# Optimization experiments

Measured on AMD Instinct MI355X. Metric: run time of the kernel, lower is better.

## Reference

```python
import jax, jax.numpy as jnp
import numpy as np

B, C_IN, C_OUT, N_LOW, N_UP, K = 16, 256, 128, 10242, 40962, 7  # ico order 5 -> 6, 1-ring size 7


def setup_inputs() -> dict:
    key = jax.random.key(0)
    k1, k2, k3 = jax.random.split(key, 3)
    x = jax.random.normal(k1, (B, C_IN, N_LOW), dtype=jnp.float32)
    # nn.Linear(in_feats, K*out_feats); stored as [in, K*out] for einsum
    weight = jax.random.normal(k2, (C_IN, K * C_OUT), dtype=jnp.float32) * 0.05
    bias = jax.random.normal(k3, (K * C_OUT,), dtype=jnp.float32) * 0.05
    # flat neighbor indices must cover every up-level vertex at least once
    rng = np.random.default_rng(0)
    cover = rng.permutation(N_UP)
    extra = rng.integers(0, N_UP, size=N_LOW * K - N_UP)
    neigh_flat = jnp.asarray(np.concatenate([cover, extra]).astype(np.int32))
    return {"x": x, "weight": weight, "bias": bias,
            "neigh_flat": neigh_flat, "n_up": N_UP}


def reference(x, weight, bias, neigh_flat, n_up):
    # x: [B, C_in, V] -> per-vertex linear expand to [B, V, K*C_out]
    Bn, _, V = x.shape
    y = jnp.einsum('bcv,cf->bvf', x, weight) + bias
    y = y.reshape(Bn, V * K, C_OUT)            # [B, V*K, C_out]
    y = jnp.transpose(y, (1, 0, 2))            # [V*K, B, C_out] segment axis first
    sums = jax.ops.segment_sum(y, neigh_flat, num_segments=n_up)      # [n_up, B, C_out]
    counts = jax.ops.segment_sum(jnp.ones((V * K,), y.dtype), neigh_flat,
                                 num_segments=n_up)                    # [n_up]
    out = sums / counts[:, None, None]         # mean over variable-size groups
    return jnp.transpose(out, (1, 2, 0))       # [B, C_out, n_up]
```

## Files before the change

kernel.cpp:

```cpp
#include <hip/hip_runtime.h>
#include <stdint.h>

#define B_    16
#define CIN   256
#define COUT  128
#define VLOW  10242
#define NUP   40962
#define KTAP  7
#define FTOT  (KTAP * COUT)
#define VK    (VLOW * KTAP)
#define NBLK  41
#define VPAD  10368
#define CSR_CAP 512

typedef __attribute__((ext_vector_type(4))) float  floatx4;
typedef __attribute__((ext_vector_type(8))) short  bf16x8;

typedef __attribute__((address_space(3))) unsigned char       lds_u8;
typedef const __attribute__((address_space(1))) unsigned char gbl_u8;

__device__ __forceinline__ void gl_lds16(const unsigned short* g, unsigned short* l) {
    __builtin_amdgcn_global_load_lds((gbl_u8*)g, (lds_u8*)l, 16, 0, 0);
}

__device__ __forceinline__ unsigned short f2bf(float f) {
    union { float f; unsigned int u; } x; x.f = f;
    unsigned int r = x.u + 0x7FFFu + ((x.u >> 16) & 1u);
    return (unsigned short)(r >> 16);
}
__device__ __forceinline__ float bflo(unsigned int u) {
    union { unsigned int u; float f; } x; x.u = u << 16; return x.f;
}
__device__ __forceinline__ float bfhi(unsigned int u) {
    union { unsigned int u; float f; } x; x.u = u & 0xFFFF0000u; return x.f;
}


__global__ void count_kernel(const int* __restrict__ neigh, int* __restrict__ counts) {
    int i = blockIdx.x * blockDim.x + threadIdx.x;
    if (i < VK) atomicAdd(&counts[neigh[i]], 1);
}

__global__ __launch_bounds__(1024)
void scan_local(const int* __restrict__ counts, int* __restrict__ offs, int* __restrict__ bsum) {
    __shared__ int s[1024];
    const int t = threadIdx.x;
    const int idx = blockIdx.x * 1024 + t;
    int v = (idx < NUP) ? counts[idx] : 0;
    s[t] = v;
    __syncthreads();
    int acc = v;
    for (int off = 1; off < 1024; off <<= 1) {
        int add = (t >= off) ? s[t - off] : 0;
        __syncthreads();
        acc += add;
        s[t] = acc;
        __syncthreads();
    }
    if (idx < NUP) offs[idx] = acc - v;
    if (t == 1023) bsum[blockIdx.x] = acc;
}

__global__ void scan_sums(const int* __restrict__ bsum, int* __restrict__ bbase) {
    __shared__ int s[64];
    int t = threadIdx.x;
    s[t] = (t < NBLK) ? bsum[t] : 0;
    __syncthreads();
    if (t == 0) {
        int r = 0;
        for (int j = 0; j < NBLK; ++j) { bbase[j] = r; r += s[j]; }
    }
}

__global__ void fill_csr(const int* __restrict__ neigh, const int* __restrict__ offs,
                         const int* __restrict__ bbase, int* __restrict__ cursor,
                         int* __restrict__ csr) {
    int i = blockIdx.x * blockDim.x + threadIdx.x;
    if (i < VK) {
        int n = neigh[i];
        int p = atomicAdd(&cursor[n], 1);
        csr[offs[n] + bbase[n >> 10] + p] = i;
    }
}

__global__ void make_pos(const int* __restrict__ offs, const int* __restrict__ bbase,
                         int* __restrict__ pos) {
    int i = blockIdx.x * blockDim.x + threadIdx.x;
    if (i <= NUP) pos[i] = (i < NUP) ? (offs[i] + bbase[i >> 10]) : VK;
}

__global__ __launch_bounds__(256)
void transpose256(const float* __restrict__ src, unsigned short* __restrict__ dst,
                  int C, int CLIM, int CPAD)
{
    __shared__ unsigned short lt[64][72];
    const int t  = threadIdx.x;
    const int v0 = blockIdx.x * 64;
    const int c0 = blockIdx.y * 64;
    const int z  = blockIdx.z;
    const float* s = src + (size_t)z * 256 * C;
    unsigned short* d = dst + (size_t)z * CPAD * 256;

#pragma unroll
    for (int p = 0; p < 16; ++p) {
        int cr = c0 + p * 4 + (t >> 6);
        int v  = v0 + (t & 63);
        float val = (v < CLIM) ? s[(size_t)cr * C + v] : 0.0f;
        lt[t & 63][p * 4 + (t >> 6)] = f2bf(val);
    }
    __syncthreads();
#pragma unroll
    for (int p = 0; p < 2; ++p) {
        int vl = p * 32 + (t >> 3);
        int v  = v0 + vl;
        if (v < CPAD) {
            uint4 val = *(const uint4*)&lt[vl][(t & 7) * 8];
            *(uint4*)&d[(size_t)v * 256 + c0 + (t & 7) * 8] = val;
        }
    }
}

__global__ __launch_bounds__(256)
void gemm_y(const unsigned short* __restrict__ xT,
            const unsigned short* __restrict__ wT,
            const float* __restrict__ bias,
            unsigned short* __restrict__ y)
{
    __shared__ unsigned short smem[16384];
    unsigned short* A0 = smem;
    unsigned short* B0 = smem + 4096;
    unsigned short* A1 = smem + 8192;
    unsigned short* B1 = smem + 12288;

    const int t    = threadIdx.x;
    const int vt   = blockIdx.x;
    const int ktap = blockIdx.y;
    const int bl   = blockIdx.z;
    const int v0   = vt * 128;
    const int f0   = ktap * 128;

    const int lane = t & 63;
    const int wid  = t >> 6;
    const int wv   = wid & 1;
    const int wf   = wid >> 1;
    const int mrow = lane & 15;
    const int quad = lane >> 4;
    const int kb   = quad * 8;

    floatx4 acc[4][4];
#pragma unroll
    for (int i = 0; i < 4; i++)
#pragma unroll
        for (int j = 0; j < 4; j++) acc[i][j] = (floatx4)0.0f;

    const int srow = (lane >> 2);
    const int scol = (lane & 3) << 3;
    const unsigned short* gA0 = xT + (((size_t)bl * VPAD + v0 + wid * 32 + srow) << 8) + scol;
    const unsigned short* gA1 = gA0 + (16 << 8);
    const unsigned short* gB0 = wT + (((size_t)f0 + wid * 32 + srow) << 8) + scol;
    const unsigned short* gB1 = gB0 + (16 << 8);
    const int woff = wid * 1024;

#define STAGE(AB, BB, KC) do {                        \
        gl_lds16(gA0 + (KC), (AB) + woff);            \
        gl_lds16(gA1 + (KC), (AB) + woff + 512);      \
        gl_lds16(gB0 + (KC), (BB) + woff);            \
        gl_lds16(gB1 + (KC), (BB) + woff + 512);      \
    } while (0)

#define COMPUTE(AB, BB) do {                                                        \
        bf16x8 fa[4], fb[4];                                                        \
        _Pragma("unroll")                                                           \
        for (int i = 0; i < 4; i++)                                                 \
            fa[i] = *(const bf16x8*)&(AB)[(wv * 64 + i * 16 + mrow) * 32 + kb];     \
        _Pragma("unroll")                                                           \
        for (int j = 0; j < 4; j++)                                                 \
            fb[j] = *(const bf16x8*)&(BB)[(wf * 64 + j * 16 + mrow) * 32 + kb];     \
        _Pragma("unroll")                                                           \
        for (int i = 0; i < 4; i++)                                                 \
            _Pragma("unroll")                                                       \
            for (int j = 0; j < 4; j++)                                             \
                acc[i][j] = __builtin_amdgcn_mfma_f32_16x16x32_bf16(fa[i], fb[j],   \
                                                                    acc[i][j], 0, 0, 0); \
    } while (0)

    STAGE(A0, B0, 0);
    __syncthreads();
#pragma unroll
    for (int tt = 0; tt < 4; ++tt) {
        const int kc = tt * 64;
        if (kc + 32 < CIN) STAGE(A1, B1, kc + 32);
        COMPUTE(A0, B0);
        __syncthreads();
        if (kc + 64 < CIN) STAGE(A0, B0, kc + 64);
        COMPUTE(A1, B1);
        __syncthreads();
    }
#undef STAGE
#undef COMPUTE

    float bvv[4];
#pragma unroll
    for (int j = 0; j < 4; j++) bvv[j] = bias[f0 + wf * 64 + j * 16 + mrow];

    unsigned short* yb = y + (size_t)bl * VLOW * FTOT;
#pragma unroll
    for (int half = 0; half < 2; ++half) {
        __syncthreads();
        if (wv == half) {
#pragma unroll
            for (int i = 0; i < 4; i++)
#pragma unroll
                for (int j = 0; j < 4; j++)
#pragma unroll
                    for (int r = 0; r < 4; r++) {
                        int vl = i * 16 + quad * 4 + r;
                        int c  = wf * 64 + j * 16 + mrow;
                        smem[vl * 130 + c] = f2bf(acc[i][j][r] + bvv[j]);
                    }
        }
        __syncthreads();
        int row = t >> 2, cb = (t & 3) * 32;
        int v = v0 + half * 64 + row;
        if (v < VLOW) {
            unsigned int tmp[16];
#pragma unroll
            for (int q = 0; q < 16; q++)
                tmp[q] = *(const unsigned int*)&smem[row * 130 + cb + q * 2];
            uint4* dst = (uint4*)(yb + (size_t)v * FTOT + f0 + cb);
            dst[0] = make_uint4(tmp[0],  tmp[1],  tmp[2],  tmp[3]);
            dst[1] = make_uint4(tmp[4],  tmp[5],  tmp[6],  tmp[7]);
            dst[2] = make_uint4(tmp[8],  tmp[9],  tmp[10], tmp[11]);
            dst[3] = make_uint4(tmp[12], tmp[13], tmp[14], tmp[15]);
        }
    }
}

__global__ __launch_bounds__(256)
void gather_out(const unsigned short* __restrict__ y, const int* __restrict__ pos,
                const int* __restrict__ csr, float* __restrict__ out)
{
    __shared__ int   s_pos[65];
    __shared__ int   s_csr[CSR_CAP];
    __shared__ float lt[64 * 130];
    const int t = threadIdx.x, lane = t & 63, wvv = t >> 6;
    const int n0 = blockIdx.x * 64;
    const int bl = blockIdx.y;
    const unsigned short* yb = y + (size_t)bl * VLOW * FTOT;

    if (t < 65) {
        int idx = n0 + t; if (idx > NUP) idx = NUP;
        s_pos[t] = pos[idx];
    }
    __syncthreads();
    const int S = s_pos[0];
    const int num = s_pos[64] - S;
    const bool fits = (num <= CSR_CAP);
    if (fits) for (int i = t; i < num; i += 256) s_csr[i] = csr[S + i];
    __syncthreads();

#pragma unroll
    for (int nl = 0; nl < 16; ++nl) {
        const int nloc = wvv * 16 + nl;
        const int st  = s_pos[nloc] - S;
        const int cnt = s_pos[nloc + 1] - s_pos[nloc];
        float a0 = 0.0f, a1 = 0.0f;
        int e = 0;
        for (; e + 2 <= cnt; e += 2) {
            int i0 = fits ? s_csr[st + e]     : csr[S + st + e];
            int i1 = fits ? s_csr[st + e + 1] : csr[S + st + e + 1];
            unsigned u0 = *(const unsigned int*)(yb + (((size_t)i0) << 7) + lane * 2);
            unsigned u1 = *(const unsigned int*)(yb + (((size_t)i1) << 7) + lane * 2);
            a0 += bflo(u0) + bflo(u1);
            a1 += bfhi(u0) + bfhi(u1);
        }
        if (e < cnt) {
            int i0 = fits ? s_csr[st + e] : csr[S + st + e];
            unsigned u0 = *(const unsigned int*)(yb + (((size_t)i0) << 7) + lane * 2);
            a0 += bflo(u0);
            a1 += bfhi(u0);
        }
        float inv = cnt ? 1.0f / (float)cnt : 0.0f;
        lt[nloc * 130 + lane * 2]     = a0 * inv;
        lt[nloc * 130 + lane * 2 + 1] = a1 * inv;
    }
    __syncthreads();

    float* ob = out + (size_t)bl * COUT * NUP;
    int nl2 = t & 63, n = n0 + nl2;
    if (n < NUP) {
#pragma unroll
        for (int rr = 0; rr < 32; ++rr) {
            int c = rr * 4 + (t >> 6);
            ob[(size_t)c * NUP + n] = lt[nl2 * 130 + c];
        }
    }
}


extern "C" void kernel_launch(void* const* d_in, const int* in_sizes, int n_in,
                              void* d_out, int out_size, void* d_ws, size_t ws_size,
                              hipStream_t stream) {
    const float* x     = (const float*)d_in[0];
    const float* w     = (const float*)d_in[1];
    const float* bias  = (const float*)d_in[2];
    const int*   neigh = (const int*)d_in[3];
    float* out = (float*)d_out;

    char* p = (char*)d_ws;
    const size_t a_nup = ((size_t)NUP * 4 + 255) & ~(size_t)255;
    int* counts = (int*)p;           p += a_nup;
    int* cursor = (int*)p;           p += a_nup;
    int* offs   = (int*)p;           p += a_nup;
    int* pos    = (int*)p;           p += a_nup + 256;
    int* bsum   = (int*)p;           p += 256;
    int* bbase  = (int*)p;           p += 256;
    int* csr    = (int*)p;           p += ((size_t)VK * 4 + 255) & ~(size_t)255;
    unsigned short* wT = (unsigned short*)p;  p += ((size_t)FTOT * 256 * 2 + 255) & ~(size_t)255;

    size_t meta    = (size_t)(p - (char*)d_ws);
    size_t xT_per  = (size_t)VPAD * 256 * 2;
    size_t y_per   = (size_t)VLOW * FTOT * 2;
    int G = 16;
    while (G > 1 && meta + (size_t)G * (xT_per + y_per) > ws_size) G >>= 1;

    unsigned short* xT = (unsigned short*)p;
    unsigned short* y  = (unsigned short*)(p + (size_t)G * xT_per);

    hipMemsetAsync(counts, 0, a_nup * 2, stream);

    count_kernel<<<(VK + 255) / 256, 256, 0, stream>>>(neigh, counts);
    scan_local<<<NBLK, 1024, 0, stream>>>(counts, offs, bsum);
    scan_sums<<<1, 64, 0, stream>>>(bsum, bbase);
    fill_csr<<<(VK + 255) / 256, 256, 0, stream>>>(neigh, offs, bbase, cursor, csr);
    make_pos<<<(NUP + 256) / 256, 256, 0, stream>>>(offs, bbase, pos);
    transpose256<<<dim3(FTOT / 64, 4, 1), 256, 0, stream>>>(w, wT, FTOT, FTOT, FTOT);

    for (int bg = 0; bg < B_; bg += G) {
        transpose256<<<dim3(VPAD / 64, 4, G), 256, 0, stream>>>(
            x + (size_t)bg * CIN * VLOW, xT, VLOW, VLOW, VPAD);
        gemm_y<<<dim3(81, KTAP, G), 256, 0, stream>>>(xT, wT, bias, y);
        gather_out<<<dim3(641, G), 256, 0, stream>>>(
            y, pos, csr, out + (size_t)bg * COUT * NUP);
    }
}
```

Before: 881.2 us.

## Stage gathered bf16 rows in swizzled LDS and write outputs directly per thread

The gather kernel now splits each 64-vertex block into two halves. For each half it cooperatively loads all referenced y rows into LDS with 16-byte loads and an XOR swizzle, then each thread reduces 16 channels for one vertex from LDS. Results go straight to the output, 32 consecutive vertices per channel, which removes the old float transpose buffer. This is meant to replace many scattered 4-byte global loads with coalesced 16-byte row loads. It adds extra barriers and falls back to direct global reads when a half has more than GCAP entries.

```diff
diff --git a/kernel.cpp b/kernel.cpp
--- a/kernel.cpp
+++ b/kernel.cpp
@@ -12,6 +12,7 @@
 #define NBLK  41
 #define VPAD  10368
 #define CSR_CAP 512
+#define GCAP  112
 
 typedef __attribute__((ext_vector_type(4))) float  floatx4;
 typedef __attribute__((ext_vector_type(8))) short  bf16x8;
@@ -242,58 +243,85 @@
 {
     __shared__ int   s_pos[65];
     __shared__ int   s_csr[CSR_CAP];
-    __shared__ float lt[64 * 130];
-    const int t = threadIdx.x, lane = t & 63, wvv = t >> 6;
+    __shared__ unsigned short s_rows[GCAP * 128];
+    const int t  = threadIdx.x;
     const int n0 = blockIdx.x * 64;
     const int bl = blockIdx.y;
     const unsigned short* yb = y + (size_t)bl * VLOW * FTOT;
+    float* ob = out + (size_t)bl * COUT * NUP;
 
     if (t < 65) {
         int idx = n0 + t; if (idx > NUP) idx = NUP;
         s_pos[t] = pos[idx];
     }
     __syncthreads();
-    const int S = s_pos[0];
+    const int S   = s_pos[0];
     const int num = s_pos[64] - S;
-    const bool fits = (num <= CSR_CAP);
-    if (fits) for (int i = t; i < num; i += 256) s_csr[i] = csr[S + i];
-    __syncthreads();
-
-#pragma unroll
-    for (int nl = 0; nl < 16; ++nl) {
-        const int nloc = wvv * 16 + nl;
-        const int st  = s_pos[nloc] - S;
-        const int cnt = s_pos[nloc + 1] - s_pos[nloc];
-        float a0 = 0.0f, a1 = 0.0f;
-        int e = 0;
-        for (; e + 2 <= cnt; e += 2) {
-            int i0 = fits ? s_csr[st + e]     : csr[S + st + e];
-            int i1 = fits ? s_csr[st + e + 1] : csr[S + st + e + 1];
-            unsigned u0 = *(const unsigned int*)(yb + (((size_t)i0) << 7) + lane * 2);
-            unsigned u1 = *(const unsigned int*)(yb + (((size_t)i1) << 7) + lane * 2);
-            a0 += bflo(u0) + bflo(u1);
-            a1 += bfhi(u0) + bfhi(u1);
-        }
-        if (e < cnt) {
-            int i0 = fits ? s_csr[st + e] : csr[S + st + e];
-            unsigned u0 = *(const unsigned int*)(yb + (((size_t)i0) << 7) + lane * 2);
-            a0 += bflo(u0);
-            a1 += bfhi(u0);
-        }
-        float inv = cnt ? 1.0f / (float)cnt : 0.0f;
-        lt[nloc * 130 + lane * 2]     = a0 * inv;
-        lt[nloc * 130 + lane * 2 + 1] = a1 * inv;
-    }
-    __syncthreads();
-
-    float* ob = out + (size_t)bl * COUT * NUP;
-    int nl2 = t & 63, n = n0 + nl2;
-    if (n < NUP) {
-#pragma unroll
-        for (int rr = 0; rr < 32; ++rr) {
-            int c = rr * 4 + (t >> 6);
-            ob[(size_t)c * NUP + n] = lt[nl2 * 130 + c];
-        }
+    const bool csr_fits = (num <= CSR_CAP);
+    if (csr_fits) for (int i = t; i < num; i += 256) s_csr[i] = csr[S + i];
+    __syncthreads();
+
+    const int nl = t & 31;
+    const int cg = t >> 5;
+
+#pragma unroll
+    for (int h = 0; h < 2; ++h) {
+        const int stH  = s_pos[h * 32] - S;
+        const int numH = s_pos[h * 32 + 32] - S - stH;
+        const bool staged = csr_fits && (numH <= GCAP);
+
+        if (staged) {
+            for (int e0 = 0; e0 < numH; e0 += 16) {
+                int e = e0 + (t >> 4);
+                if (e < numH) {
+                    int i = s_csr[stH + e];
+                    uint4 d = *(const uint4*)(yb + (((size_t)i) << 7) + (t & 15) * 8);
+                    int cq = ((t & 15) * 4) ^ ((e & 15) << 2);
+                    *(uint4*)((char*)s_rows + e * 256 + cq * 4) = d;
+                }
+            }
+        }
+        __syncthreads();
+
+        const int nloc = h * 32 + nl;
+        const int stN  = s_pos[nloc] - S;
+        const int cnt  = s_pos[nloc + 1] - s_pos[nloc];
+        float acc[16];
+#pragma unroll
+        for (int k = 0; k < 16; ++k) acc[k] = 0.0f;
+
+        for (int e = 0; e < cnt; ++e) {
+            uint4 d0, d1;
+            if (staged) {
+                int r   = stN - stH + e;
+                int cq0 = (cg * 8)     ^ ((r & 15) << 2);
+                int cq1 = (cg * 8 + 4) ^ ((r & 15) << 2);
+                d0 = *(const uint4*)((const char*)s_rows + r * 256 + cq0 * 4);
+                d1 = *(const uint4*)((const char*)s_rows + r * 256 + cq1 * 4);
+            } else {
+                int i = csr_fits ? s_csr[stN + e] : csr[S + stN + e];
+                const unsigned short* row = yb + (((size_t)i) << 7);
+                d0 = *(const uint4*)(row + cg * 16);
+                d1 = *(const uint4*)(row + cg * 16 + 8);
+            }
+            acc[0]  += bflo(d0.x); acc[1]  += bfhi(d0.x);
+            acc[2]  += bflo(d0.y); acc[3]  += bfhi(d0.y);
+            acc[4]  += bflo(d0.z); acc[5]  += bfhi(d0.z);
+            acc[6]  += bflo(d0.w); acc[7]  += bfhi(d0.w);
+            acc[8]  += bflo(d1.x); acc[9]  += bfhi(d1.x);
+            acc[10] += bflo(d1.y); acc[11] += bfhi(d1.y);
+            acc[12] += bflo(d1.z); acc[13] += bfhi(d1.z);
+            acc[14] += bflo(d1.w); acc[15] += bfhi(d1.w);
+        }
+
+        int n = n0 + nloc;
+        if (n < NUP) {
+            float inv = cnt ? 1.0f / (float)cnt : 0.0f;
+#pragma unroll
+            for (int k = 0; k < 16; ++k)
+                ob[(size_t)(cg * 16 + k) * NUP + n] = acc[k] * inv;
+        }
+        __syncthreads();
     }
 }
 
```

Measured after the change: 850.7 us. 1.04x faster.
